# Performance work log

Measured on AMD Instinct MI355X. Metric: run time of the kernel, lower is better.

Reference implementation:

```python
import jax, jax.numpy as jnp
import numpy as np


def setup_inputs() -> dict:
    key = jax.random.key(0)
    ks = jax.random.split(key, 8)
    B, T, C = 8, 2048, 1024
    X = jax.random.normal(ks[0], (B, T, C), dtype=jnp.float32)
    dX = jax.random.normal(ks[1], (B, T, C), dtype=jnp.float32)
    S_n = jnp.zeros((B, C), dtype=jnp.float32)
    att_mask = jnp.ones((B, T), dtype=jnp.int64)
    # parameters (torch init: randn(C,C)/C ; nn.Linear default uniform)
    W_Q = jax.random.normal(ks[2], (C, C), dtype=jnp.float32) / C
    W_K = jax.random.normal(ks[3], (C, C), dtype=jnp.float32) / C
    W_V = jax.random.normal(ks[4], (C, C), dtype=jnp.float32) / C
    bound = 1.0 / np.sqrt(C)
    W_hh = jax.random.uniform(ks[5], (C, C), minval=-bound, maxval=bound, dtype=jnp.float32)
    b_hh = jax.random.uniform(ks[6], (C,), minval=-bound, maxval=bound, dtype=jnp.float32)
    return {"X": X, "dX": dX, "S_n": S_n, "att_mask": att_mask,
            "W_Q": W_Q, "W_K": W_K, "W_V": W_V, "W_hh": W_hh, "b_hh": b_hh}


def reference(X, dX, S_n, att_mask, W_Q, W_K, W_V, W_hh, b_hh):
    B, T, C = X.shape
    # chunk_len is hard-coded to 1 in the source, so per-step:
    #   Q_t,K_t,V_t: [B,1,C]; c_t = Q_t @ K_t^T: [B,1,1]; A_t = c_t @ V_t.
    # These have no cross-timestep dependency -> precompute in parallel.
    Q = jax.nn.relu(jnp.einsum('btc,cd->btd', X, W_Q))
    K = jax.nn.relu(jnp.einsum('btc,cd->btd', X, W_K))
    V = jnp.einsum('btc,cd->btd', X, W_V)
    s = jnp.sum(Q * K, axis=-1, keepdims=True)        # [B,T,1]
    A = s * V                                          # [B,T,C]
    # A_factor = A_scale[chunk_len-1] = linspace(0,-1,ceil(T/2))[0] == 0.0
    A_scale = jnp.concatenate([jnp.linspace(0.0, -1.0, (T + 1) // 2),
                               jnp.linspace(-1.0, 0.0, T // 2)])
    A_factor = A_scale[0]

    def step(carry, A_t):
        h, prev_A = carry
        h_new = jnp.tanh(h @ W_hh.T + b_hh + A_t + prev_A * A_factor)
        return (h_new, A_t), h_new

    h0 = jnp.zeros((B, C), X.dtype)
    A_seq = jnp.swapaxes(A, 0, 1)                      # [T,B,C]
    _, H = jax.lax.scan(step, (h0, h0), A_seq)
    out = jnp.swapaxes(H, 0, 1)                        # [B,T,C]
    return out, S_n
```

## Files before the change

kernel.cpp:

```cpp
#include <hip/hip_runtime.h>
#include <hip/hip_bf16.h>

#define Bn 8
#define Tn 2048
#define Cn 1024

typedef __attribute__((ext_vector_type(8))) short short8;
typedef __attribute__((ext_vector_type(4))) float f32x4;

__device__ __forceinline__ unsigned short f2bf(float x) {
    union { float f; unsigned u; } v; v.f = x;
    return (unsigned short)((v.u + 0x7FFFu + ((v.u >> 16) & 1u)) >> 16);
}

__global__ __launch_bounds__(256) void transpose_cvt(const float* __restrict__ W,
                                                     unsigned short* __restrict__ WT) {
    __shared__ float tile[64][65];
    const int bx = blockIdx.x;
    const int tr = (bx >> 4) << 6;
    const int tc = (bx & 15) << 6;
    const int tid = threadIdx.x;
    const int r  = tid >> 2;
    const int c4 = (tid & 3) << 4;
#pragma unroll
    for (int i = 0; i < 4; ++i) {
        float4 v = *(const float4*)(W + (long)(tr + r) * Cn + tc + c4 + i * 4);
        tile[r][c4 + i * 4 + 0] = v.x;
        tile[r][c4 + i * 4 + 1] = v.y;
        tile[r][c4 + i * 4 + 2] = v.z;
        tile[r][c4 + i * 4 + 3] = v.w;
    }
    __syncthreads();
    short8 p0, p1;
#pragma unroll
    for (int i = 0; i < 8; ++i)  p0[i] = (short)f2bf(tile[c4 + i][r]);
#pragma unroll
    for (int i = 0; i < 8; ++i)  p1[i] = (short)f2bf(tile[c4 + 8 + i][r]);
    unsigned short* dst = WT + (long)(tc + r) * Cn + tr + c4;
    *(short8*)(dst)     = p0;
    *(short8*)(dst + 8) = p1;
}

__global__ __launch_bounds__(256, 1) void qkv_fused(const float* __restrict__ X,
                                                    const unsigned short* __restrict__ WqT,
                                                    const unsigned short* __restrict__ WkT,
                                                    const unsigned short* __restrict__ WvT,
                                                    float* __restrict__ Aout) {
    extern __shared__ char smem[];
    char* xs = smem;
    char* b0 = smem + 131072;
    char* b1 = smem + 147456;
    const int tid = threadIdx.x;
    const long row0 = (long)blockIdx.x * 64;

#pragma unroll 4
    for (int it = 0; it < 32; ++it) {
        int chunk = it * 256 + tid;
        int r  = chunk >> 7;
        int cc = chunk & 127;
        const float* src = X + (row0 + r) * Cn + cc * 8;
        float4 v0 = *(const float4*)src;
        float4 v1 = *(const float4*)(src + 4);
        short8 p;
        p[0] = (short)f2bf(v0.x); p[1] = (short)f2bf(v0.y);
        p[2] = (short)f2bf(v0.z); p[3] = (short)f2bf(v0.w);
        p[4] = (short)f2bf(v1.x); p[5] = (short)f2bf(v1.y);
        p[6] = (short)f2bf(v1.z); p[7] = (short)f2bf(v1.w);
        *(short8*)(xs + r * 2048 + ((cc * 16) ^ ((r & 7) << 4))) = p;
    }

    const int lane = tid & 63;
    const int wv   = tid >> 6;
    const int wm   = wv & 1;
    const int wn   = wv >> 1;
    const int m0   = wm * 32;
    const int l15  = lane & 15;
    const int lk   = lane >> 4;

    float s_part[2][4] = {};

    for (int nb = 0; nb < 8; ++nb) {
        const int n0 = nb * 128;
        f32x4 qa[2][4] = {};
        f32x4 ka[2][4] = {};
        for (int k0 = 0; k0 < 16; ++k0) {
            const int kk = k0 * 64;
            __syncthreads();
#pragma unroll
            for (int i = 0; i < 4; ++i) {
                int ch = i * 256 + tid;
                int n  = ch >> 3;
                int s  = ch & 7;
                int loff = n * 128 + ((s * 16) ^ ((n & 7) << 4));
                long goff = (long)(n0 + n) * Cn + kk + s * 8;
                *(short8*)(b0 + loff) = *(const short8*)(WqT + goff);
                *(short8*)(b1 + loff) = *(const short8*)(WkT + goff);
            }
            __syncthreads();
#pragma unroll
            for (int ki = 0; ki < 2; ++ki) {
                const int kb  = (kk + ki * 32 + lk * 8) * 2;
                const int r0  = m0 + l15, r1 = m0 + 16 + l15;
                short8 a0 = *(const short8*)(xs + r0 * 2048 + (kb ^ ((r0 & 7) << 4)));
                short8 a1 = *(const short8*)(xs + r1 * 2048 + (kb ^ ((r1 & 7) << 4)));
                const int bkb = (ki * 32 + lk * 8) * 2;
#pragma unroll
                for (int nf = 0; nf < 4; ++nf) {
                    int n = wn * 64 + nf * 16 + l15;
                    int boff = n * 128 + (bkb ^ ((n & 7) << 4));
                    short8 bq = *(const short8*)(b0 + boff);
                    qa[0][nf] = __builtin_amdgcn_mfma_f32_16x16x32_bf16(a0, bq, qa[0][nf], 0, 0, 0);
                    qa[1][nf] = __builtin_amdgcn_mfma_f32_16x16x32_bf16(a1, bq, qa[1][nf], 0, 0, 0);
                    short8 bk = *(const short8*)(b1 + boff);
                    ka[0][nf] = __builtin_amdgcn_mfma_f32_16x16x32_bf16(a0, bk, ka[0][nf], 0, 0, 0);
                    ka[1][nf] = __builtin_amdgcn_mfma_f32_16x16x32_bf16(a1, bk, ka[1][nf], 0, 0, 0);
                }
            }
        }
#pragma unroll
        for (int mf = 0; mf < 2; ++mf)
#pragma unroll
            for (int nf = 0; nf < 4; ++nf)
#pragma unroll
                for (int r = 0; r < 4; ++r) {
                    float q = fmaxf(qa[mf][nf][r], 0.f);
                    float k = fmaxf(ka[mf][nf][r], 0.f);
                    s_part[mf][r] += q * k;
                }
    }
#pragma unroll
    for (int mf = 0; mf < 2; ++mf)
#pragma unroll
        for (int r = 0; r < 4; ++r) {
            float v = s_part[mf][r];
            v += __shfl_xor(v, 1);
            v += __shfl_xor(v, 2);
            v += __shfl_xor(v, 4);
            v += __shfl_xor(v, 8);
            s_part[mf][r] = v;
        }

    {
        float* s_red = (float*)b1;
        if (l15 == 0) {
#pragma unroll
            for (int mf = 0; mf < 2; ++mf)
#pragma unroll
                for (int r = 0; r < 4; ++r)
                    s_red[wn * 64 + m0 + mf * 16 + lk * 4 + r] = s_part[mf][r];
        }
        __syncthreads();
#pragma unroll
        for (int mf = 0; mf < 2; ++mf)
#pragma unroll
            for (int r = 0; r < 4; ++r) {
                int row = m0 + mf * 16 + lk * 4 + r;
                s_part[mf][r] = s_red[row] + s_red[64 + row];
            }
        __syncthreads();
    }

    for (int nb = 0; nb < 8; ++nb) {
        const int n0 = nb * 128;
        f32x4 va[2][4] = {};
        for (int k0 = 0; k0 < 16; ++k0) {
            const int kk = k0 * 64;
            __syncthreads();
#pragma unroll
            for (int i = 0; i < 4; ++i) {
                int ch = i * 256 + tid;
                int n  = ch >> 3;
                int s  = ch & 7;
                *(short8*)(b0 + n * 128 + ((s * 16) ^ ((n & 7) << 4))) =
                    *(const short8*)(WvT + (long)(n0 + n) * Cn + kk + s * 8);
            }
            __syncthreads();
#pragma unroll
            for (int ki = 0; ki < 2; ++ki) {
                const int kb  = (kk + ki * 32 + lk * 8) * 2;
                const int r0  = m0 + l15, r1 = m0 + 16 + l15;
                short8 a0 = *(const short8*)(xs + r0 * 2048 + (kb ^ ((r0 & 7) << 4)));
                short8 a1 = *(const short8*)(xs + r1 * 2048 + (kb ^ ((r1 & 7) << 4)));
                const int bkb = (ki * 32 + lk * 8) * 2;
#pragma unroll
                for (int nf = 0; nf < 4; ++nf) {
                    int n = wn * 64 + nf * 16 + l15;
                    short8 bv = *(const short8*)(b0 + n * 128 + (bkb ^ ((n & 7) << 4)));
                    va[0][nf] = __builtin_amdgcn_mfma_f32_16x16x32_bf16(a0, bv, va[0][nf], 0, 0, 0);
                    va[1][nf] = __builtin_amdgcn_mfma_f32_16x16x32_bf16(a1, bv, va[1][nf], 0, 0, 0);
                }
            }
        }
#pragma unroll
        for (int mf = 0; mf < 2; ++mf)
#pragma unroll
            for (int nf = 0; nf < 4; ++nf)
#pragma unroll
                for (int r = 0; r < 4; ++r) {
                    long row = row0 + m0 + mf * 16 + lk * 4 + r;
                    int  col = n0 + wn * 64 + nf * 16 + l15;
                    Aout[row * Cn + col] = s_part[mf][r] * va[mf][nf][r];
                }
    }
}

#define CK(x, bit, vv)                                                        \
    if ((pend & (bit)) && (unsigned)((x) >> 32) == expect) {                  \
        vv = __uint_as_float((unsigned)(x)); pend &= ~(bit);                  \
    }

__global__ __launch_bounds__(256, 2)
void recurrence(const float* __restrict__ A,
                const float* __restrict__ Whh,
                const float* __restrict__ bhh,
                unsigned long long* __restrict__ cbuf,
                float* __restrict__ out) {
    const int tid = threadIdx.x;
    const int b   = blockIdx.x & 7;
    const int sl  = blockIdx.x >> 3;
    const int j0  = sl * 32;
    const int j   = tid & 31;
    const int ch  = tid >> 5;

    __shared__ float sbuf[16000];
    float* h_lds = sbuf;
    float* part  = sbuf + 1024;

    float4 w[32];
    const float4* wp = (const float4*)(Whh + (long)(j0 + j) * Cn + ch * 128);
#pragma unroll
    for (int r = 0; r < 32; ++r) w[r] = wp[r];
#pragma unroll
    for (int r = 0; r < 32; ++r) {
        asm volatile("" : "+v"(w[r].x), "+v"(w[r].y), "+v"(w[r].z), "+v"(w[r].w));
    }

    const float bh = (tid < 32) ? bhh[j0 + tid] : 0.f;

    for (int t = 1; t <= Tn; ++t) {
        float a_val = 0.f;
        if (tid < 32) a_val = A[((long)b * Tn + (t - 1)) * Cn + j0 + tid];

        unsigned long long* src =
            cbuf + ((size_t)((t - 1) & 1) * Bn + b) * Cn + tid * 4;
        const unsigned expect = (unsigned)(t - 1);
        float v0 = 0.f, v1 = 0.f, v2 = 0.f, v3 = 0.f;
        unsigned pend = 0xF;
        unsigned long long a0, a1, a2, a3;
        do {
            asm volatile(
                "global_load_dwordx2 %0, %4, off sc0\n\t"
                "global_load_dwordx2 %1, %4, off offset:8 sc0\n\t"
                "global_load_dwordx2 %2, %4, off offset:16 sc0\n\t"
                "global_load_dwordx2 %3, %4, off offset:24 sc0\n\t"
                "s_waitcnt vmcnt(0)"
                : "=&v"(a0), "=&v"(a1), "=&v"(a2), "=&v"(a3)
                : "v"(src) : "memory");
            CK(a0, 1u, v0) CK(a1, 2u, v1) CK(a2, 4u, v2) CK(a3, 8u, v3)
            if (!pend) break;
            asm volatile(
                "global_load_dwordx2 %0, %4, off sc0 sc1\n\t"
                "global_load_dwordx2 %1, %4, off offset:8 sc0 sc1\n\t"
                "global_load_dwordx2 %2, %4, off offset:16 sc0 sc1\n\t"
                "global_load_dwordx2 %3, %4, off offset:24 sc0 sc1\n\t"
                "s_waitcnt vmcnt(0)"
                : "=&v"(a0), "=&v"(a1), "=&v"(a2), "=&v"(a3)
                : "v"(src) : "memory");
            CK(a0, 1u, v0) CK(a1, 2u, v1) CK(a2, 4u, v2) CK(a3, 8u, v3)
        } while (pend);
        *(float4*)(h_lds + tid * 4) = make_float4(v0, v1, v2, v3);
        __syncthreads();

        float ax = 0.f, ay = 0.f, az = 0.f, aw = 0.f;
#pragma unroll
        for (int r = 0; r < 32; ++r) {
            float4 h4 = *(const float4*)(h_lds + ch * 128 + r * 4);
            ax = fmaf(w[r].x, h4.x, ax);
            ay = fmaf(w[r].y, h4.y, ay);
            az = fmaf(w[r].z, h4.z, az);
            aw = fmaf(w[r].w, h4.w, aw);
        }
        part[ch * 32 + j] = (ax + ay) + (az + aw);
        __syncthreads();

        if (tid < 32) {
            float s = 0.f;
#pragma unroll
            for (int c = 0; c < 8; ++c) s += part[c * 32 + tid];
            float ht = tanhf(s + a_val + bh);
            unsigned long long pk =
                ((unsigned long long)(unsigned)t << 32) | (unsigned long long)__float_as_uint(ht);
            unsigned long long* dst =
                cbuf + ((size_t)(t & 1) * Bn + b) * Cn + j0 + tid;
            asm volatile(
                "global_store_dwordx2 %0, %1, off sc0\n\t"
                "global_store_dwordx2 %0, %1, off sc0 sc1"
                :: "v"(dst), "v"(pk) : "memory");
            out[((long)b * Tn + (t - 1)) * Cn + j0 + tid] = ht;
        }
        __syncthreads();
    }
}

extern "C" void kernel_launch(void* const* d_in, const int* in_sizes, int n_in,
                              void* d_out, int out_size, void* d_ws, size_t ws_size,
                              hipStream_t stream) {
    const float* X   = (const float*)d_in[0];
    const float* S_n = (const float*)d_in[2];
    const float* W_Q = (const float*)d_in[4];
    const float* W_K = (const float*)d_in[5];
    const float* W_V = (const float*)d_in[6];
    const float* Whh = (const float*)d_in[7];
    const float* bhh = (const float*)d_in[8];
    float* out = (float*)d_out;

    char* ws = (char*)d_ws;
    float*              A     = (float*)ws;
    unsigned short*     WqT   = (unsigned short*)(ws + 67108864);
    unsigned short*     WkT   = WqT + 1024 * 1024;
    unsigned short*     WvT   = WkT + 1024 * 1024;
    unsigned long long* cbuf  = (unsigned long long*)(ws + 67108864 + 3 * 2097152);

    (void)hipFuncSetAttribute((const void*)qkv_fused,
                              hipFuncAttributeMaxDynamicSharedMemorySize, 163840);

    (void)hipMemsetAsync(cbuf, 0, 2 * Bn * Cn * sizeof(unsigned long long), stream);

    transpose_cvt<<<256, 256, 0, stream>>>(W_Q, WqT);
    transpose_cvt<<<256, 256, 0, stream>>>(W_K, WkT);
    transpose_cvt<<<256, 256, 0, stream>>>(W_V, WvT);

    qkv_fused<<<256, 256, 163840, stream>>>(X, WqT, WkT, WvT, A);

    recurrence<<<256, 256, 0, stream>>>(A, Whh, bhh, cbuf, out);

    (void)hipMemcpyAsync(out + (long)Bn * Tn * Cn, S_n, Bn * Cn * sizeof(float),
                         hipMemcpyDeviceToDevice, stream);
}
```

Baseline: 4.500 ms.

## Cut per-step barriers in recurrence, widen poll loads, use fast tanh

The recurrence loop drops two of its three block-wide barriers per timestep. Each wave reads back only the hidden-state slice it wrote itself, so an LDS waitcnt is enough, and the partial-sum buffer is double-buffered by timestep parity. The cross-block flag polling now uses two 16-byte loads instead of four 8-byte loads. tanhf is replaced with an exp and reciprocal formulation. The aim is to shorten the serial per-step latency of the 2048-step recurrence, at some cost in tanh accuracy and a reliance on the wave-local data layout.

```diff
diff --git a/kernel.cpp b/kernel.cpp
--- a/kernel.cpp
+++ b/kernel.cpp
@@ -7,6 +7,7 @@
 
 typedef __attribute__((ext_vector_type(8))) short short8;
 typedef __attribute__((ext_vector_type(4))) float f32x4;
+typedef __attribute__((ext_vector_type(4))) unsigned int u32x4;
 
 __device__ __forceinline__ unsigned short f2bf(float x) {
     union { float f; unsigned u; } v; v.f = x;
@@ -204,9 +205,9 @@
     }
 }
 
-#define CK(x, bit, vv)                                                        \
-    if ((pend & (bit)) && (unsigned)((x) >> 32) == expect) {                  \
-        vv = __uint_as_float((unsigned)(x)); pend &= ~(bit);                  \
+#define CK(tag, dat, bit, vv)                                                 \
+    if ((pend & (bit)) && (tag) == expect) {                                  \
+        vv = __uint_as_float(dat); pend &= ~(bit);                            \
     }
 
 __global__ __launch_bounds__(256, 2)
@@ -224,7 +225,7 @@
 
     __shared__ float sbuf[16000];
     float* h_lds = sbuf;
-    float* part  = sbuf + 1024;
+    float* part2 = sbuf + 1024;
 
     float4 w[32];
     const float4* wp = (const float4*)(Whh + (long)(j0 + j) * Cn + ch * 128);
@@ -246,30 +247,28 @@
         const unsigned expect = (unsigned)(t - 1);
         float v0 = 0.f, v1 = 0.f, v2 = 0.f, v3 = 0.f;
         unsigned pend = 0xF;
-        unsigned long long a0, a1, a2, a3;
+        u32x4 pa, pb;
         do {
             asm volatile(
-                "global_load_dwordx2 %0, %4, off sc0\n\t"
-                "global_load_dwordx2 %1, %4, off offset:8 sc0\n\t"
-                "global_load_dwordx2 %2, %4, off offset:16 sc0\n\t"
-                "global_load_dwordx2 %3, %4, off offset:24 sc0\n\t"
+                "global_load_dwordx4 %0, %2, off sc0\n\t"
+                "global_load_dwordx4 %1, %2, off offset:16 sc0\n\t"
                 "s_waitcnt vmcnt(0)"
-                : "=&v"(a0), "=&v"(a1), "=&v"(a2), "=&v"(a3)
-                : "v"(src) : "memory");
-            CK(a0, 1u, v0) CK(a1, 2u, v1) CK(a2, 4u, v2) CK(a3, 8u, v3)
+                : "=&v"(pa), "=&v"(pb) : "v"(src) : "memory");
+            CK(pa.y, pa.x, 1u, v0) CK(pa.w, pa.z, 2u, v1)
+            CK(pb.y, pb.x, 4u, v2) CK(pb.w, pb.z, 8u, v3)
             if (!pend) break;
             asm volatile(
-                "global_load_dwordx2 %0, %4, off sc0 sc1\n\t"
-                "global_load_dwordx2 %1, %4, off offset:8 sc0 sc1\n\t"
-                "global_load_dwordx2 %2, %4, off offset:16 sc0 sc1\n\t"
-                "global_load_dwordx2 %3, %4, off offset:24 sc0 sc1\n\t"
+                "global_load_dwordx4 %0, %2, off sc0 sc1\n\t"
+                "global_load_dwordx4 %1, %2, off offset:16 sc0 sc1\n\t"
                 "s_waitcnt vmcnt(0)"
-                : "=&v"(a0), "=&v"(a1), "=&v"(a2), "=&v"(a3)
-                : "v"(src) : "memory");
-            CK(a0, 1u, v0) CK(a1, 2u, v1) CK(a2, 4u, v2) CK(a3, 8u, v3)
+                : "=&v"(pa), "=&v"(pb) : "v"(src) : "memory");
+            CK(pa.y, pa.x, 1u, v0) CK(pa.w, pa.z, 2u, v1)
+            CK(pb.y, pb.x, 4u, v2) CK(pb.w, pb.z, 8u, v3)
         } while (pend);
+
         *(float4*)(h_lds + tid * 4) = make_float4(v0, v1, v2, v3);
-        __syncthreads();
+        asm volatile("s_waitcnt lgkmcnt(0)" ::: "memory");
+        __builtin_amdgcn_sched_barrier(0);
 
         float ax = 0.f, ay = 0.f, az = 0.f, aw = 0.f;
 #pragma unroll
@@ -280,14 +279,16 @@
             az = fmaf(w[r].z, h4.z, az);
             aw = fmaf(w[r].w, h4.w, aw);
         }
-        part[ch * 32 + j] = (ax + ay) + (az + aw);
+        part2[(t & 1) * 256 + ch * 32 + j] = (ax + ay) + (az + aw);
         __syncthreads();
 
         if (tid < 32) {
-            float s = 0.f;
-#pragma unroll
-            for (int c = 0; c < 8; ++c) s += part[c * 32 + tid];
-            float ht = tanhf(s + a_val + bh);
+            const float* pp = part2 + (t & 1) * 256;
+            float s = ((pp[tid] + pp[32 + tid]) + (pp[64 + tid] + pp[96 + tid])) +
+                      ((pp[128 + tid] + pp[160 + tid]) + (pp[192 + tid] + pp[224 + tid]));
+            float x = s + a_val + bh;
+            float e = __expf(x + x);
+            float ht = 1.f - 2.f * __builtin_amdgcn_rcpf(e + 1.f);
             unsigned long long pk =
                 ((unsigned long long)(unsigned)t << 32) | (unsigned long long)__float_as_uint(ht);
             unsigned long long* dst =
@@ -298,7 +299,6 @@
                 :: "v"(dst), "v"(pk) : "memory");
             out[((long)b * Tn + (t - 1)) * Cn + j0 + tid] = ht;
         }
-        __syncthreads();
     }
 }
 
```

Measured after the change: 4.581 ms. About the same (+1.8%).
